# Optimization experiments

Measured on AMD Instinct MI355X. Metric: run time of the kernel, lower is better.

The kernel has to match this reference:

```python
import jax, jax.numpy as jnp
import numpy as np

H, HD, NKV = 16, 128, 4           # heads, head_dim, n_kv_heads (kv_groups=4)
SEL_TOPK, SEL_DIM, SEL_HEADS = 64, 64, 1
ROPE_BASE = 10000.0


def _rope_emb(t, hd):
    inv = 1.0 / (ROPE_BASE ** (jnp.arange(0, hd, 2, dtype=jnp.float32) / hd))
    freqs = jnp.arange(t, dtype=jnp.float32)[:, None] * inv[None, :]
    return jnp.concatenate([freqs, freqs], axis=-1)  # [t, hd]


def _apply_rotary(x, rope):
    # x: [b, t, h, hd]; rope: [t, hd] (rot_dim == hd here)
    cos = jnp.cos(rope)[None, :, None, :]
    sin = jnp.sin(rope)[None, :, None, :]
    x1, x2 = x[..., ::2], x[..., 1::2]
    c, s = cos[..., ::2], sin[..., ::2]
    rot = jnp.stack([x1 * c - x2 * s, x1 * s + x2 * c], axis=-1)
    return rot.reshape(x.shape)


def _selector_mask(q, k):
    # q, k: [b, H, t, hd] in UNrotated form (selector_rope='none'); causal=True
    b, h, t, d = q.shape
    qs = q[:, :SEL_HEADS, :, :SEL_DIM]
    ks = k[:, :SEL_HEADS, :, :SEL_DIM]
    scores = jnp.einsum('bhqd,bhkd->bhqk', qs, ks) / np.sqrt(SEL_DIM).astype(np.float32)
    future = jnp.triu(jnp.ones((t, t), bool), 1)
    scores = jnp.where(future[None, None], -jnp.inf, scores)
    idx = jax.lax.top_k(scores, SEL_TOPK)[1]  # [b, h_sel, t, keep]
    rows = jnp.arange(t)
    scatter_row = lambda im: jnp.zeros((t, t), bool).at[rows[:, None], im].set(True)
    sel = jax.vmap(jax.vmap(scatter_row))(idx)          # [b, h_sel, t, t]
    sel = sel.at[:, :, rows, rows].set(True)            # diagonal always kept
    sel = sel & jnp.tril(jnp.ones((t, t), bool))[None, None]
    sel = jnp.any(sel, axis=1, keepdims=True)           # h_sel < h -> broadcast mask
    return jnp.where(sel, 0.0, -jnp.inf).astype(jnp.float32)


def reference(x, Wq, bq, Wkd, bkd, Wku, bku, Wo, bo):
    b, t, d = x.shape
    G = H // NKV
    q = (x @ Wq + bq).reshape(b, t, H, HD)
    kv = (x @ Wkd + bkd) @ Wku + bku                    # MLA: down then up projection
    k = kv[..., : NKV * HD].reshape(b, t, NKV, HD)
    v = kv[..., NKV * HD:].reshape(b, t, NKV, HD)
    rope = _rope_emb(t, HD)
    qb = _apply_rotary(q, rope).transpose(0, 2, 1, 3)                     # [b,H,t,hd]
    kb = jnp.repeat(_apply_rotary(k, rope).transpose(0, 2, 1, 3), G, 1)   # GQA expand
    vb = jnp.repeat(v.transpose(0, 2, 1, 3), G, 1)
    # selector mask from unrotated q/k, detached (selector_detach=True)
    qu = jax.lax.stop_gradient(q.transpose(0, 2, 1, 3))
    ku = jnp.repeat(jax.lax.stop_gradient(k.transpose(0, 2, 1, 3)), G, 1)
    mask = _selector_mask(qu, ku)                                         # [b,1,t,t]
    scores = jnp.einsum('bhqd,bhkd->bhqk', qb, kb) / np.sqrt(HD).astype(np.float32)
    attn = jax.nn.softmax(scores + mask, axis=-1)
    y = jnp.einsum('bhqk,bhkd->bhqd', attn, vb)
    y = y.transpose(0, 2, 1, 3).reshape(b, t, H * HD)
    return y @ Wo + bo


def setup_inputs() -> dict:
    key = jax.random.key(0)
    ks = jax.random.split(key, 6)
    B, T, D, LAT = 2, 2048, 2048, 512
    s = 0.02
    return {
        'x': jax.random.normal(ks[0], (B, T, D), jnp.float32),
        'Wq': jax.random.normal(ks[1], (D, H * HD), jnp.float32) * s,
        'bq': jnp.zeros((H * HD,), jnp.float32),
        'Wkd': jax.random.normal(ks[2], (D, LAT), jnp.float32) * s,
        'bkd': jnp.zeros((LAT,), jnp.float32),
        'Wku': jax.random.normal(ks[3], (LAT, 2 * NKV * HD), jnp.float32) * s,
        'bku': jnp.zeros((2 * NKV * HD,), jnp.float32),
        'Wo': jax.random.normal(ks[4], (H * HD, D), jnp.float32) * s,
        'bo': jnp.zeros((D,), jnp.float32),
    }
```

## Files before the change

### kernel.cpp

```cpp
#include <hip/hip_runtime.h>

typedef unsigned int u32;
typedef unsigned long long u64;
typedef _Float16 f16;
typedef __attribute__((ext_vector_type(2))) _Float16 f16x2;
typedef __attribute__((ext_vector_type(4))) _Float16 f16x4;
typedef __attribute__((ext_vector_type(8))) _Float16 f16x8;
typedef __attribute__((ext_vector_type(4))) float f32x4;
typedef __attribute__((ext_vector_type(2))) double f64x2;


__device__ __forceinline__ int suX(int jj) { return jj ^ ((jj >> 4) & 7); }

__global__ __launch_bounds__(256) void k_transpose_cast(const float* __restrict__ in,
                                                        f16* __restrict__ out, int R, int C)
{
  __shared__ float tile[32][33];
  int c0 = blockIdx.x * 32, r0 = blockIdx.y * 32;
  int tx = threadIdx.x & 31, ty = threadIdx.x >> 5;
  #pragma unroll
  for (int i = ty; i < 32; i += 8) tile[i][tx] = in[(size_t)(r0 + i) * C + c0 + tx];
  __syncthreads();
  #pragma unroll
  for (int i = ty; i < 32; i += 8) out[(size_t)(c0 + i) * R + r0 + tx] = (f16)tile[tx][i];
}

__global__ __launch_bounds__(256) void k_cast_f16(const float* __restrict__ in,
                                                  f16* __restrict__ out, int n4)
{
  int i = blockIdx.x * 256 + threadIdx.x;
  if (i >= n4) return;
  f32x4 v = *(const f32x4*)&in[(size_t)i * 4];
  f16x4 h; h.x = (f16)v.x; h.y = (f16)v.y; h.z = (f16)v.z; h.w = (f16)v.w;
  *(f16x4*)&out[(size_t)i * 4] = h;
}

__global__ void k_prep_sel(const float* __restrict__ Wq, const float* __restrict__ Wkd,
                           const float* __restrict__ Wku, double* __restrict__ Bsel)
{
  const int k = blockIdx.x;
  const int j = threadIdx.x;
  Bsel[(size_t)k * 128 + j] = (double)Wq[(size_t)k * 2048 + j];
  double s = 0.0;
  for (int l = 0; l < 512; ++l)
    s = fma((double)Wkd[(size_t)k * 512 + l], (double)Wku[(size_t)l * 1024 + j], s);
  Bsel[(size_t)k * 128 + 64 + j] = s;
}

__global__ void k_bias_sel(const float* __restrict__ bq, const float* __restrict__ bkd,
                           const float* __restrict__ Wku, const float* __restrict__ bku,
                           double* __restrict__ bsel)
{
  int j = threadIdx.x;
  if (j < 64) {
    bsel[j] = (double)bq[j];
  } else {
    int jj = j - 64;
    double s = (double)bku[jj];
    for (int l = 0; l < 512; ++l)
      s = fma((double)bkd[l], (double)Wku[(size_t)l * 1024 + jj], s);
    bsel[j] = s;
  }
}

__global__ __launch_bounds__(256) void k_gemm_sel_f64(const float* __restrict__ A,
                                                      const double* __restrict__ Bsel,
                                                      double* __restrict__ partial)
{
  __shared__ double As[32][33];
  __shared__ double Bs[32][66];
  const int m0 = blockIdx.x * 32, n0 = blockIdx.y * 64;
  const int kbase = blockIdx.z * 512, kend = kbase + 512;
  const int tid = threadIdx.x;
  const int tx = tid & 15, ty = tid >> 4;
  const int ar = tid >> 3, ac4 = (tid & 7) * 4;
  double acc[2][4] = {};

  f32x4 aN = *(const f32x4*)&A[(size_t)(m0 + ar) * 2048 + kbase + ac4];
  f64x2 bN[4];
  #pragma unroll
  for (int it = 0; it < 4; ++it) {
    int c = it * 256 + tid; int kk = c >> 5, n2 = (c & 31) * 2;
    bN[it] = *(const f64x2*)&Bsel[(size_t)(kbase + kk) * 128 + n0 + n2];
  }
  for (int k0 = kbase; k0 < kend; k0 += 32) {
    __syncthreads();
    As[ar][ac4] = (double)aN.x; As[ar][ac4 + 1] = (double)aN.y;
    As[ar][ac4 + 2] = (double)aN.z; As[ar][ac4 + 3] = (double)aN.w;
    #pragma unroll
    for (int it = 0; it < 4; ++it) {
      int c = it * 256 + tid; int kk = c >> 5, n2 = (c & 31) * 2;
      Bs[kk][n2] = bN[it].x; Bs[kk][n2 + 1] = bN[it].y;
    }
    __syncthreads();
    if (k0 + 32 < kend) {
      aN = *(const f32x4*)&A[(size_t)(m0 + ar) * 2048 + k0 + 32 + ac4];
      #pragma unroll
      for (int it = 0; it < 4; ++it) {
        int c = it * 256 + tid; int kk = c >> 5, n2 = (c & 31) * 2;
        bN[it] = *(const f64x2*)&Bsel[(size_t)(k0 + 32 + kk) * 128 + n0 + n2];
      }
    }
    #pragma unroll
    for (int kk = 0; kk < 32; ++kk) {
      double a0 = As[ty * 2][kk], a1 = As[ty * 2 + 1][kk];
      f64x2 b01 = *(const f64x2*)&Bs[kk][tx * 4];
      f64x2 b23 = *(const f64x2*)&Bs[kk][tx * 4 + 2];
      acc[0][0] = fma(a0, b01.x, acc[0][0]); acc[0][1] = fma(a0, b01.y, acc[0][1]);
      acc[0][2] = fma(a0, b23.x, acc[0][2]); acc[0][3] = fma(a0, b23.y, acc[0][3]);
      acc[1][0] = fma(a1, b01.x, acc[1][0]); acc[1][1] = fma(a1, b01.y, acc[1][1]);
      acc[1][2] = fma(a1, b23.x, acc[1][2]); acc[1][3] = fma(a1, b23.y, acc[1][3]);
    }
  }
  double* op = partial + (size_t)blockIdx.z * 4096 * 128;
  #pragma unroll
  for (int i = 0; i < 2; ++i) {
    int row = m0 + ty * 2 + i;
    #pragma unroll
    for (int j = 0; j < 4; ++j) {
      int n = n0 + tx * 4 + j;
      op[(size_t)row * 128 + n] = acc[i][j];
    }
  }
}

__global__ __launch_bounds__(256) void k_sel_reduce(const double* __restrict__ partial,
                                                    const double* __restrict__ bias,
                                                    double* __restrict__ qs64,
                                                    double* __restrict__ ks64)
{
  const int idx = blockIdx.x * 256 + threadIdx.x;
  const int row = idx >> 7, n = idx & 127;
  const size_t S = 4096 * 128;
  double v = ((partial[idx] + partial[S + idx]) + partial[2 * S + idx]) + partial[3 * S + idx];
  v += bias[n];
  if (n < 64) qs64[(size_t)row * 64 + n] = v;
  else        ks64[(size_t)row * 64 + (n - 64)] = v;
}

__global__ __launch_bounds__(256) void k_transpose64(const double* __restrict__ in,
                                                     double* __restrict__ out)
{
  __shared__ double tile[32][33];
  const int bt = blockIdx.z;
  const int c0 = blockIdx.x * 32;
  const int r0 = blockIdx.y * 32;
  int tx = threadIdx.x & 31, ty = threadIdx.x >> 5;
  const double* ip = in + (size_t)bt * 2048 * 64;
  double* op = out + (size_t)bt * 64 * 2048;
  #pragma unroll
  for (int i = ty; i < 32; i += 8) tile[i][tx] = ip[(size_t)(r0 + i) * 64 + c0 + tx];
  __syncthreads();
  #pragma unroll
  for (int i = ty; i < 32; i += 8) op[(size_t)(c0 + i) * 2048 + r0 + tx] = tile[tx][i];
}

template <bool OUTF16>
__global__ __launch_bounds__(256) void k_gemm_bt(const f16* __restrict__ A,
                                                 const f16* __restrict__ BT,
                                                 const float* __restrict__ bias,
                                                 float* __restrict__ C, f16* __restrict__ Ch,
                                                 int M, int N, int K, int lda, int ldb, int ldc)
{
  __shared__ __align__(16) f16 As[128 * 64];
  __shared__ __align__(16) f16 Bs[128 * 64];
  const int tid = threadIdx.x;
  const int lane = tid & 63;
  const int wave = tid >> 6;
  const int m0 = blockIdx.x * 128, n0 = blockIdx.y * 128;
  const int wr = (wave >> 1) * 64, wc = (wave & 1) * 64;
  const int lrow = lane & 15;
  const int kgrp = (lane >> 4) * 8;
  f32x4 acc[4][4] = {};

  for (int k0 = 0; k0 < K; k0 += 64) {
    __syncthreads();
    #pragma unroll
    for (int it = 0; it < 4; ++it) {
      int c = it * 256 + tid;
      int r = c >> 3, c8 = (c & 7) * 8;
      int lbase = (it * 256 + (tid & 192)) * 8;
      const f16* ga = A + (size_t)(m0 + r) * lda + k0 + c8;
      __builtin_amdgcn_global_load_lds((const __attribute__((address_space(1))) u32*)ga,
                                       (__attribute__((address_space(3))) u32*)&As[lbase],
                                       16, 0, 0);
      const f16* gb = BT + (size_t)(n0 + r) * ldb + k0 + c8;
      __builtin_amdgcn_global_load_lds((const __attribute__((address_space(1))) u32*)gb,
                                       (__attribute__((address_space(3))) u32*)&Bs[lbase],
                                       16, 0, 0);
    }
    __syncthreads();
    #pragma unroll
    for (int ks = 0; ks < 2; ++ks) {
      f16x8 af[4], bfr[4];
      #pragma unroll
      for (int m = 0; m < 4; ++m)
        af[m] = *(const f16x8*)&As[(wr + m * 16 + lrow) * 64 + ks * 32 + kgrp];
      #pragma unroll
      for (int n = 0; n < 4; ++n)
        bfr[n] = *(const f16x8*)&Bs[(wc + n * 16 + lrow) * 64 + ks * 32 + kgrp];
      #pragma unroll
      for (int m = 0; m < 4; ++m)
        #pragma unroll
        for (int n = 0; n < 4; ++n)
          acc[m][n] = __builtin_amdgcn_mfma_f32_16x16x32_f16(af[m], bfr[n], acc[m][n], 0, 0, 0);
    }
  }
  const int rbase = m0 + wr + (lane >> 4) * 4;
  #pragma unroll
  for (int n = 0; n < 4; ++n) {
    int col = n0 + wc + n * 16 + lrow;
    float bv = bias ? bias[col] : 0.0f;
    #pragma unroll
    for (int m = 0; m < 4; ++m) {
      #pragma unroll
      for (int j = 0; j < 4; ++j) {
        int rowi = rbase + m * 16 + j;
        float v = acc[m][n][j] + bv;
        if (OUTF16) Ch[(size_t)rowi * ldc + col] = (f16)v;
        else        C[(size_t)rowi * ldc + col] = v;
      }
    }
  }
}

__global__ void k_rope_table(float* __restrict__ rc, float* __restrict__ rs)
{
  int t = blockIdx.x, i = threadIdx.x;
  int fi = (2 * i) & 63;
  double inv = pow(10000.0, -(double)fi / 64.0);
  double a = (double)t * inv;
  rc[t * 64 + i] = (float)cos(a);
  rs[t * 64 + i] = (float)sin(a);
}

__global__ __launch_bounds__(256) void k_rope_q(const f16* __restrict__ q,
                                                const float* __restrict__ rc,
                                                const float* __restrict__ rs,
                                                f16* __restrict__ out)
{
  int g = blockIdx.x * 256 + threadIdx.x;
  int row = g >> 10, rem = g & 1023;
  int h = rem >> 6, i = rem & 63;
  int t = row & 2047;
  size_t base = (size_t)row * 2048 + h * 128 + 2 * i;
  f16x2 v = *(const f16x2*)&q[base];
  float x1 = (float)v.x, x2 = (float)v.y;
  float c = rc[t * 64 + i], s = rs[t * 64 + i];
  f16x2 o; o.x = (f16)(x1 * c - x2 * s); o.y = (f16)(x1 * s + x2 * c);
  *(f16x2*)&out[base] = o;
}

__global__ __launch_bounds__(256) void k_rope_kv(const f16* __restrict__ kv,
                                                 const float* __restrict__ rc,
                                                 const float* __restrict__ rs,
                                                 f16* __restrict__ kout, f16* __restrict__ vout)
{
  int g = blockIdx.x * 256 + threadIdx.x;
  int row = g >> 8, rem = g & 255;
  int kvh = rem >> 6, i = rem & 63;
  int t = row & 2047;
  size_t kb = (size_t)row * 1024 + kvh * 128 + 2 * i;
  f16x2 kvp = *(const f16x2*)&kv[kb];
  float x1 = (float)kvp.x, x2 = (float)kvp.y;
  float c = rc[t * 64 + i], s = rs[t * 64 + i];
  size_t ob = (size_t)row * 512 + kvh * 128 + 2 * i;
  f16x2 ko; ko.x = (f16)(x1 * c - x2 * s); ko.y = (f16)(x1 * s + x2 * c);
  *(f16x2*)&kout[ob] = ko;
  f16x2 vp = *(const f16x2*)&kv[(size_t)row * 1024 + 512 + kvh * 128 + 2 * i];
  *(f16x2*)&vout[ob] = vp;
}

__global__ __launch_bounds__(256) void k_topk64(const double* __restrict__ qs,
                                                const double* __restrict__ ksT,
                                                int* __restrict__ selcnt,
                                                int* __restrict__ selidx)
{
  const int r0 = blockIdx.x * 2;
  const int b = r0 >> 11;
  const int t0 = r0 & 2047, t1 = t0 + 1;
  const int tid = threadIdx.x;
  if (t1 < 64) {
    for (int lr = 0; lr < 2; ++lr) {
      int t = t0 + lr;
      int* outp = selidx + (size_t)(r0 + lr) * 68;
      for (int jj = tid; jj <= t; jj += 256) outp[jj] = jj;
      if (tid == 0) selcnt[r0 + lr] = t + 1;
    }
    return;
  }
  __shared__ double qrowP[64][2];
  __shared__ u64 su[2][2048];
  __shared__ unsigned hist[256], sA[256], sB[256];
  __shared__ unsigned s_bsel, s_larger, s_cnt;
  __shared__ u64 s_thr;
  __shared__ int s_remfin;
  __shared__ int cand[128];
  __shared__ u64 ckey[128];

  if (tid < 128) qrowP[tid >> 1][tid & 1] = qs[(size_t)(r0 + (tid & 1)) * 64 + (tid >> 1)];
  __syncthreads();
  {
    const double* kb = ksT + (size_t)b * 64 * 2048;
    const int emax = t1 >> 8;
    for (int e = 0; e <= emax; ++e) {
      const int jj = e * 256 + tid;
      double acc0 = 0.0, acc1 = 0.0;
      const double* kp = kb + jj;
      #pragma unroll 16
      for (int d = 0; d < 64; ++d) {
        double kv = kp[(size_t)d * 2048];
        f64x2 qp = *(const f64x2*)&qrowP[d][0];
        acc0 = fma(qp.x, kv, acc0);
        acc1 = fma(qp.y, kv, acc1);
      }
      const int sx = suX(jj);
      u64 u0 = (u64)__double_as_longlong(acc0);
      su[0][sx] = (u0 >> 63) ? ~u0 : (u0 | 0x8000000000000000ull);
      u64 u1 = (u64)__double_as_longlong(acc1);
      su[1][sx] = (u1 >> 63) ? ~u1 : (u1 | 0x8000000000000000ull);
    }
  }
  __syncthreads();

  const int c0 = tid * 8;
  for (int lr = 0; lr < 2; ++lr) {
    const int t = t0 + lr;
    int* outp = selidx + (size_t)(r0 + lr) * 68;
    const u64* S = su[lr];
    u64 prefix = 0;
    int remaining = 64;
    int broke = 0, sh_final = 0;
    for (int byte = 7; byte >= 0; --byte) {
      const int sh = byte * 8;
      hist[tid] = 0;
      __syncthreads();
      {
        unsigned bn[8]; bool vl[8];
        #pragma unroll
        for (int e = 0; e < 8; ++e) {
          int jj = c0 + e;
          u64 u = (jj <= t) ? S[suX(jj)] : 0;
          bool ok = (jj <= t) && ((byte == 7) || (((u ^ prefix) >> (sh + 8)) == 0));
          bn[e] = (unsigned)((u >> sh) & 255);
          vl[e] = ok;
        }
        #pragma unroll
        for (int e = 0; e < 8; ++e) {
          if (vl[e]) {
            bool first = true;
            #pragma unroll
            for (int p = 0; p < 8; ++p)
              if (p < e && vl[p] && bn[p] == bn[e]) first = false;
            if (first) {
              unsigned c = 0;
              #pragma unroll
              for (int q = 0; q < 8; ++q)
                if (q >= e && vl[q] && bn[q] == bn[e]) ++c;
              atomicAdd(&hist[bn[e]], c);
            }
          }
        }
      }
      __syncthreads();
      unsigned* sp = sA; unsigned* dp = sB;
      sp[tid] = hist[tid];
      __syncthreads();
      #pragma unroll
      for (int off = 1; off < 256; off <<= 1) {
        dp[tid] = sp[tid] + ((tid + off < 256) ? sp[tid + off] : 0u);
        __syncthreads();
        unsigned* tpp = sp; sp = dp; dp = tpp;
      }
      unsigned inc = sp[tid];
      unsigned cumAbove = (tid == 255) ? 0u : sp[tid + 1];
      if ((int)cumAbove < remaining && (int)inc >= remaining) {
        s_bsel = (unsigned)tid;
        s_larger = cumAbove;
        s_cnt = inc - cumAbove;
      }
      __syncthreads();
      prefix |= ((u64)s_bsel << sh);
      remaining -= (int)s_larger;
      int cnt = (int)s_cnt;
      __syncthreads();
      if (cnt <= 128) { broke = 1; sh_final = sh; break; }
    }
    u64 thr;
    int remfin;
    if (broke) {
      unsigned cg = 0;
      #pragma unroll
      for (int e = 0; e < 8; ++e) {
        int jj = c0 + e;
        if (jj <= t && (((S[suX(jj)] ^ prefix) >> sh_final) == 0)) ++cg;
      }
      unsigned* sp = sA; unsigned* dp = sB;
      sp[tid] = cg;
      __syncthreads();
      #pragma unroll
      for (int off = 1; off < 256; off <<= 1) {
        dp[tid] = sp[tid] + ((tid >= off) ? sp[tid - off] : 0u);
        __syncthreads();
        unsigned* tpp = sp; sp = dp; dp = tpp;
      }
      const int C = (int)sp[255];
      int pos = (int)(sp[tid] - cg);
      #pragma unroll
      for (int e = 0; e < 8; ++e) {
        int jj = c0 + e;
        if (jj <= t && (((S[suX(jj)] ^ prefix) >> sh_final) == 0)) cand[pos++] = jj;
      }
      __syncthreads();
      if (tid < C) ckey[tid] = S[suX(cand[tid])];
      __syncthreads();
      if (tid < C) {
        u64 k = ckey[tid];
        int g = 0, eq = 0;
        for (int j = 0; j < C; ++j) {
          g += (ckey[j] > k) ? 1 : 0;
          eq += (ckey[j] == k) ? 1 : 0;
        }
        if (g < remaining && remaining <= g + eq) {
          s_thr = k;
          s_remfin = remaining - g;
        }
      }
      __syncthreads();
      thr = s_thr;
      remfin = s_remfin;
    } else {
      thr = prefix;
      remfin = remaining;
    }
    __syncthreads();
    unsigned cg = 0, ct_ = 0;
    #pragma unroll
    for (int e = 0; e < 8; ++e) {
      int jj = c0 + e;
      if (jj <= t) {
        u64 u = S[suX(jj)];
        cg += (u > thr) ? 1u : 0u;
        ct_ += (u == thr) ? 1u : 0u;
      }
    }
    const unsigned pack = cg | (ct_ << 16);
    {
      unsigned* sp = sA; unsigned* dp = sB;
      sp[tid] = pack;
      __syncthreads();
      #pragma unroll
      for (int off = 1; off < 256; off <<= 1) {
        dp[tid] = sp[tid] + ((tid >= off) ? sp[tid - off] : 0u);
        __syncthreads();
        unsigned* tpp = sp; sp = dp; dp = tpp;
      }
      const unsigned excl = sp[tid] - pack;
      const unsigned tot = sp[255];
      const unsigned Gtot = tot & 0xFFFFu;
      const u64 ut = S[suX(t)];
      const unsigned gt = (ut > thr) ? 1u : 0u;
      const unsigned tt = (ut == thr) ? 1u : 0u;
      const int GtotX = (int)(Gtot - gt);
      int gpos = (int)(excl & 0xFFFFu);
      int tpos = (int)(excl >> 16);
      #pragma unroll
      for (int e = 0; e < 8; ++e) {
        int jj = c0 + e;
        if (jj > t) break;
        u64 u = S[suX(jj)];
        if (u > thr) {
          if (jj != t) outp[1 + gpos] = jj;
          ++gpos;
        } else if (u == thr) {
          if (jj != t && tpos < remfin) outp[1 + GtotX + tpos] = jj;
          ++tpos;
        }
      }
      if (tid == 0) {
        outp[0] = t;
        const unsigned Ttot = tot >> 16;
        int tb = (int)(Ttot - tt);
        int emitT = tb < remfin ? tb : remfin;
        selcnt[r0 + lr] = 1 + GtotX + emitT;
      }
    }
    __syncthreads();
  }
}

__global__ __launch_bounds__(256) void k_attn(const f16* __restrict__ qr,
                                              const f16* __restrict__ kr,
                                              const f16* __restrict__ vv,
                                              const int* __restrict__ selcnt,
                                              const int* __restrict__ selidx,
                                              f16* __restrict__ y)
{
  const int blk = blockIdx.x;
  const int row = blk >> 2, kvh = blk & 3;
  const int b = row >> 11;
  const int tid = threadIdx.x, lane = tid & 63, wave = tid >> 6;
  const int cnt = selcnt[row];
  __shared__ int sidx[68];
  __shared__ __align__(16) f16 Kl[65 * 128];
  __shared__ __align__(16) f16 Vl[65 * 128];
  __shared__ f16 qlds[4][128];
  __shared__ float pl[4][66];
  if (tid < cnt) sidx[tid] = selidx[(size_t)row * 68 + tid];
  *(f16x2*)&qlds[wave][lane * 2] =
      *(const f16x2*)&qr[((size_t)row * 16 + kvh * 4 + wave) * 128 + lane * 2];
  __syncthreads();

  const int nch = cnt * 16;
  for (int c = tid; c < nch; c += 256) {
    const int r = c >> 4, ch = c & 15;
    const size_t kbase = ((size_t)(b * 2048 + sidx[r])) * 512 + kvh * 128 + ch * 8;
    f16x8 k8 = *(const f16x8*)&kr[kbase];
    *(f16x8*)&Kl[r * 128 + ((ch ^ (r & 15)) * 8)] = k8;
    f16x8 v8 = *(const f16x8*)&vv[kbase];
    *(f16x8*)&Vl[r * 128 + ch * 8] = v8;
  }
  __syncthreads();

  const float SCALE = 0.08838834764831845f;
  auto dotk = [&](int r) -> float {
    const int sw = r & 15;
    float s = 0.0f;
    #pragma unroll
    for (int i = 0; i < 16; ++i) {
      f16x8 k8 = *(const f16x8*)&Kl[r * 128 + ((i ^ sw) * 8)];
      f16x8 q8 = *(const f16x8*)&qlds[wave][i * 8];
      #pragma unroll
      for (int e = 0; e < 4; ++e) {
        f16x2 ka; ka.x = k8[2 * e]; ka.y = k8[2 * e + 1];
        f16x2 qa; qa.x = q8[2 * e]; qa.y = q8[2 * e + 1];
        s = __builtin_amdgcn_fdot2(ka, qa, s, false);
      }
    }
    return s * SCALE;
  };

  float s1 = -__builtin_inff(), s2 = -__builtin_inff();
  if (lane < cnt) s1 = dotk(lane);
  if (lane + 64 < cnt) s2 = dotk(lane + 64);
  float mx = fmaxf(s1, s2);
  #pragma unroll
  for (int off = 32; off; off >>= 1) mx = fmaxf(mx, __shfl_xor(mx, off));
  float p1 = (lane < cnt) ? __expf(s1 - mx) : 0.0f;
  float p2 = (lane + 64 < cnt) ? __expf(s2 - mx) : 0.0f;
  float l = p1 + p2;
  #pragma unroll
  for (int off = 32; off; off >>= 1) l += __shfl_xor(l, off);
  float linv = 1.0f / l;
  pl[wave][lane] = p1;
  if (lane == 0) pl[wave][64] = p2;
  __syncthreads();

  float y0 = 0.0f, y1 = 0.0f;
  const int d2 = lane * 2;
  for (int j = 0; j < cnt; ++j) {
    float p = pl[wave][j];
    f16x2 v2 = *(const f16x2*)&Vl[j * 128 + d2];
    y0 = fmaf(p, (float)v2.x, y0);
    y1 = fmaf(p, (float)v2.y, y1);
  }
  y0 *= linv; y1 *= linv;
  f16x2 o; o.x = (f16)y0; o.y = (f16)y1;
  *(f16x2*)&y[(size_t)row * 2048 + (kvh * 4 + wave) * 128 + d2] = o;
}

extern "C" void kernel_launch(void* const* d_in, const int* in_sizes, int n_in,
                              void* d_out, int out_size, void* d_ws, size_t ws_size,
                              hipStream_t stream)
{
  (void)in_sizes; (void)n_in; (void)out_size; (void)ws_size;
  const float* x   = (const float*)d_in[0];
  const float* Wq  = (const float*)d_in[1];
  const float* bq  = (const float*)d_in[2];
  const float* Wkd = (const float*)d_in[3];
  const float* bkd = (const float*)d_in[4];
  const float* Wku = (const float*)d_in[5];
  const float* bku = (const float*)d_in[6];
  const float* Wo  = (const float*)d_in[7];
  const float* bo  = (const float*)d_in[8];
  float* out = (float*)d_out;

  char* ws = (char*)d_ws;
  size_t o = 0;
  auto alloc = [&](size_t bytes) -> void* {
    o = (o + 255) & ~(size_t)255;
    void* p = ws + o;
    o += bytes;
    return p;
  };
  f16* WqT   = (f16*)alloc(2048ull * 2048 * 2);
  f16* WoT   = (f16*)alloc(2048ull * 2048 * 2);
  f16* WkdT  = (f16*)alloc(512ull * 2048 * 2);
  f16* WkuT  = (f16*)alloc(1024ull * 512 * 2);
  f16* xh    = (f16*)alloc(4096ull * 2048 * 2);
  f16* qmain = (f16*)alloc(4096ull * 2048 * 2);
  f16* kvh_  = (f16*)alloc(4096ull * 1024 * 2);
  f16* cbf   = (f16*)alloc(4096ull * 512 * 2);
  float* rc  = (float*)alloc(2048ull * 64 * 4);
  float* rs  = (float*)alloc(2048ull * 64 * 4);
  f16* qrope = (f16*)alloc(4096ull * 2048 * 2);
  f16* krope = (f16*)alloc(4096ull * 512 * 2);
  f16* vbf   = (f16*)alloc(4096ull * 512 * 2);
  int* selcnt = (int*)alloc(4096ull * 4);
  int* selidx = (int*)alloc(4096ull * 68 * 4);
  double* Bsel = (double*)alloc(2048ull * 128 * 8);
  double* bsel = (double*)alloc(128 * 8);
  double* qs64 = (double*)alloc(4096ull * 64 * 8);
  double* ks64 = (double*)alloc(4096ull * 64 * 8);
  double* ksT  = (double*)alloc(2ull * 64 * 2048 * 8);
  f16* yh = qmain;
  double* partial = (double*)qrope;

  k_transpose_cast<<<dim3(64, 64), 256, 0, stream>>>(Wq, WqT, 2048, 2048);
  k_transpose_cast<<<dim3(16, 64), 256, 0, stream>>>(Wkd, WkdT, 2048, 512);
  k_transpose_cast<<<dim3(32, 16), 256, 0, stream>>>(Wku, WkuT, 512, 1024);
  k_transpose_cast<<<dim3(64, 64), 256, 0, stream>>>(Wo, WoT, 2048, 2048);
  k_cast_f16<<<8192, 256, 0, stream>>>(x, xh, 2097152);

  k_prep_sel<<<2048, 64, 0, stream>>>(Wq, Wkd, Wku, Bsel);
  k_bias_sel<<<1, 128, 0, stream>>>(bq, bkd, Wku, bku, bsel);
  k_gemm_sel_f64<<<dim3(128, 2, 4), 256, 0, stream>>>(x, Bsel, partial);
  k_sel_reduce<<<2048, 256, 0, stream>>>(partial, bsel, qs64, ks64);
  k_transpose64<<<dim3(2, 64, 2), 256, 0, stream>>>(ks64, ksT);

  k_gemm_bt<true><<<dim3(32, 16), 256, 0, stream>>>(xh, WqT, bq, nullptr, qmain,
                                                    4096, 2048, 2048, 2048, 2048, 2048);
  k_gemm_bt<true><<<dim3(32, 4), 256, 0, stream>>>(xh, WkdT, bkd, nullptr, cbf,
                                                   4096, 512, 2048, 2048, 2048, 512);
  k_gemm_bt<true><<<dim3(32, 8), 256, 0, stream>>>(cbf, WkuT, bku, nullptr, kvh_,
                                                   4096, 1024, 512, 512, 512, 1024);

  k_rope_table<<<2048, 64, 0, stream>>>(rc, rs);
  k_rope_q<<<16384, 256, 0, stream>>>(qmain, rc, rs, qrope);
  k_rope_kv<<<4096, 256, 0, stream>>>(kvh_, rc, rs, krope, vbf);

  k_topk64<<<2048, 256, 0, stream>>>(qs64, ksT, selcnt, selidx);

  k_attn<<<16384, 256, 0, stream>>>(qrope, krope, vbf, selcnt, selidx, yh);

  k_gemm_bt<false><<<dim3(32, 16), 256, 0, stream>>>(yh, WoT, bo, out, nullptr,
                                                     4096, 2048, 2048, 2048, 2048, 2048);
}
```

Baseline: 537.9 us.

## Use MFMA for sparse attention QK and PV in k_attn

Rewrites the per-row sparse attention kernel to compute the 4 query heads of a KV group against the selected keys with 16x16x32 f16 MFMA instructions instead of per-lane fdot2 loops. V is held in registers, then transposed into the shared buffer that held K, with an XOR swizzle, so that P·V also runs on MFMA. Probabilities are normalized and stored as f16 in a padded buffer. This adds LDS transpose work, wastes 12 of the 16 MFMA rows, and lowers precision by rounding P to f16.

```diff
diff --git a/kernel.cpp b/kernel.cpp
--- a/kernel.cpp
+++ b/kernel.cpp
@@ -502,71 +502,129 @@
   const int tid = threadIdx.x, lane = tid & 63, wave = tid >> 6;
   const int cnt = selcnt[row];
   __shared__ int sidx[68];
-  __shared__ __align__(16) f16 Kl[65 * 128];
-  __shared__ __align__(16) f16 Vl[65 * 128];
-  __shared__ f16 qlds[4][128];
-  __shared__ float pl[4][66];
+  __shared__ __align__(16) f16 KV[13312];
+  __shared__ __align__(16) f16 Pbuf[16 * 104];
   if (tid < cnt) sidx[tid] = selidx[(size_t)row * 68 + tid];
-  *(f16x2*)&qlds[wave][lane * 2] =
-      *(const f16x2*)&qr[((size_t)row * 16 + kvh * 4 + wave) * 128 + lane * 2];
   __syncthreads();
 
-  const int nch = cnt * 16;
-  for (int c = tid; c < nch; c += 256) {
+  for (int c = tid; c < cnt * 16; c += 256) {
     const int r = c >> 4, ch = c & 15;
-    const size_t kbase = ((size_t)(b * 2048 + sidx[r])) * 512 + kvh * 128 + ch * 8;
-    f16x8 k8 = *(const f16x8*)&kr[kbase];
-    *(f16x8*)&Kl[r * 128 + ((ch ^ (r & 15)) * 8)] = k8;
-    f16x8 v8 = *(const f16x8*)&vv[kbase];
-    *(f16x8*)&Vl[r * 128 + ch * 8] = v8;
-  }
+    f16x8 k8 = *(const f16x8*)&kr[((size_t)(b * 2048 + sidx[r])) * 512 + kvh * 128 + ch * 8];
+    *(f16x8*)&KV[r * 128 + ((ch ^ (r & 15)) * 8)] = k8;
+  }
+  f16x8 vreg[6];
+  #pragma unroll
+  for (int it = 0; it < 6; ++it) {
+    const int c = it * 256 + tid;
+    const int r = c >> 4, ch = c & 15;
+    f16x8 z = {};
+    if (r < cnt)
+      z = *(const f16x8*)&vv[((size_t)(b * 2048 + sidx[r])) * 512 + kvh * 128 + ch * 8];
+    vreg[it] = z;
+  }
+  for (int i = tid; i < 16 * 104 / 2; i += 256) ((u32*)Pbuf)[i] = 0u;
+  const f16* qb = qr + (size_t)row * 2048 + (4 * kvh + (lane & 3)) * 128;
+  f16x8 qf[4];
+  #pragma unroll
+  for (int k0 = 0; k0 < 4; ++k0) qf[k0] = *(const f16x8*)&qb[k0 * 32 + (lane >> 4) * 8];
   __syncthreads();
 
+  f32x4 sc[5];
+  #pragma unroll
+  for (int n = 0; n < 5; ++n) {
+    f32x4 a = {0.f, 0.f, 0.f, 0.f};
+    const int r = n * 16 + (lane & 15);
+    #pragma unroll
+    for (int k0 = 0; k0 < 4; ++k0) {
+      const int ch = (k0 * 4 + (lane >> 4)) ^ (r & 15);
+      f16x8 bf = *(const f16x8*)&KV[r * 128 + ch * 8];
+      a = __builtin_amdgcn_mfma_f32_16x16x32_f16(qf[k0], bf, a, 0, 0, 0);
+    }
+    sc[n] = a;
+  }
   const float SCALE = 0.08838834764831845f;
-  auto dotk = [&](int r) -> float {
-    const int sw = r & 15;
-    float s = 0.0f;
-    #pragma unroll
-    for (int i = 0; i < 16; ++i) {
-      f16x8 k8 = *(const f16x8*)&Kl[r * 128 + ((i ^ sw) * 8)];
-      f16x8 q8 = *(const f16x8*)&qlds[wave][i * 8];
-      #pragma unroll
-      for (int e = 0; e < 4; ++e) {
-        f16x2 ka; ka.x = k8[2 * e]; ka.y = k8[2 * e + 1];
-        f16x2 qa; qa.x = q8[2 * e]; qa.y = q8[2 * e + 1];
-        s = __builtin_amdgcn_fdot2(ka, qa, s, false);
-      }
-    }
-    return s * SCALE;
-  };
-
-  float s1 = -__builtin_inff(), s2 = -__builtin_inff();
-  if (lane < cnt) s1 = dotk(lane);
-  if (lane + 64 < cnt) s2 = dotk(lane + 64);
-  float mx = fmaxf(s1, s2);
-  #pragma unroll
-  for (int off = 32; off; off >>= 1) mx = fmaxf(mx, __shfl_xor(mx, off));
-  float p1 = (lane < cnt) ? __expf(s1 - mx) : 0.0f;
-  float p2 = (lane + 64 < cnt) ? __expf(s2 - mx) : 0.0f;
-  float l = p1 + p2;
-  #pragma unroll
-  for (int off = 32; off; off >>= 1) l += __shfl_xor(l, off);
-  float linv = 1.0f / l;
-  pl[wave][lane] = p1;
-  if (lane == 0) pl[wave][64] = p2;
+  const float NINF = -__builtin_inff();
+  float ps[5][4];
+  float mx0 = NINF, mx1 = NINF, mx2 = NINF, mx3 = NINF;
+  #pragma unroll
+  for (int n = 0; n < 5; ++n) {
+    const bool ok = (n * 16 + (lane & 15)) < cnt;
+    #pragma unroll
+    for (int j = 0; j < 4; ++j) ps[n][j] = ok ? sc[n][j] * SCALE : NINF;
+    mx0 = fmaxf(mx0, ps[n][0]); mx1 = fmaxf(mx1, ps[n][1]);
+    mx2 = fmaxf(mx2, ps[n][2]); mx3 = fmaxf(mx3, ps[n][3]);
+  }
+  #pragma unroll
+  for (int off = 1; off < 16; off <<= 1) {
+    mx0 = fmaxf(mx0, __shfl_xor(mx0, off)); mx1 = fmaxf(mx1, __shfl_xor(mx1, off));
+    mx2 = fmaxf(mx2, __shfl_xor(mx2, off)); mx3 = fmaxf(mx3, __shfl_xor(mx3, off));
+  }
+  float l0 = 0.f, l1 = 0.f, l2 = 0.f, l3 = 0.f;
+  #pragma unroll
+  for (int n = 0; n < 5; ++n) {
+    ps[n][0] = __expf(ps[n][0] - mx0); l0 += ps[n][0];
+    ps[n][1] = __expf(ps[n][1] - mx1); l1 += ps[n][1];
+    ps[n][2] = __expf(ps[n][2] - mx2); l2 += ps[n][2];
+    ps[n][3] = __expf(ps[n][3] - mx3); l3 += ps[n][3];
+  }
+  #pragma unroll
+  for (int off = 1; off < 16; off <<= 1) {
+    l0 += __shfl_xor(l0, off); l1 += __shfl_xor(l1, off);
+    l2 += __shfl_xor(l2, off); l3 += __shfl_xor(l3, off);
+  }
+  const float i0 = 1.f / l0, i1 = 1.f / l1, i2 = 1.f / l2, i3 = 1.f / l3;
+  if (lane < 16) {
+    #pragma unroll
+    for (int n = 0; n < 5; ++n) {
+      const int key = n * 16 + lane;
+      Pbuf[0 * 104 + key] = (f16)(ps[n][0] * i0);
+      Pbuf[1 * 104 + key] = (f16)(ps[n][1] * i1);
+      Pbuf[2 * 104 + key] = (f16)(ps[n][2] * i2);
+      Pbuf[3 * 104 + key] = (f16)(ps[n][3] * i3);
+    }
+  }
   __syncthreads();
 
-  float y0 = 0.0f, y1 = 0.0f;
-  const int d2 = lane * 2;
-  for (int j = 0; j < cnt; ++j) {
-    float p = pl[wave][j];
-    f16x2 v2 = *(const f16x2*)&Vl[j * 128 + d2];
-    y0 = fmaf(p, (float)v2.x, y0);
-    y1 = fmaf(p, (float)v2.y, y1);
-  }
-  y0 *= linv; y1 *= linv;
-  f16x2 o; o.x = (f16)y0; o.y = (f16)y1;
-  *(f16x2*)&y[(size_t)row * 2048 + (kvh * 4 + wave) * 128 + d2] = o;
+  #pragma unroll
+  for (int it = 0; it < 6; ++it) {
+    const int c = it * 256 + tid;
+    const int r = c >> 4, ch = c & 15;
+    #pragma unroll
+    for (int e = 0; e < 8; ++e) {
+      const int d = ch * 8 + e;
+      const int rs = (r < 64) ? (r ^ (((d >> 3) & 7) << 3)) : r;
+      KV[d * 104 + rs] = vreg[it][e];
+    }
+  }
+  __syncthreads();
+
+  f32x4 ov0 = {0.f, 0.f, 0.f, 0.f}, ov1 = {0.f, 0.f, 0.f, 0.f};
+  #pragma unroll
+  for (int k0 = 0; k0 < 3; ++k0) {
+    f16x8 pa = *(const f16x8*)&Pbuf[(lane & 15) * 104 + k0 * 32 + (lane >> 4) * 8];
+    const int g = k0 * 4 + (lane >> 4);
+    const int rbase = g * 8;
+    {
+      const int d = wave * 32 + (lane & 15);
+      const int rs = (rbase < 64) ? (rbase ^ (((d >> 3) & 7) << 3)) : rbase;
+      f16x8 vb = *(const f16x8*)&KV[d * 104 + rs];
+      ov0 = __builtin_amdgcn_mfma_f32_16x16x32_f16(pa, vb, ov0, 0, 0, 0);
+    }
+    {
+      const int d = wave * 32 + 16 + (lane & 15);
+      const int rs = (rbase < 64) ? (rbase ^ (((d >> 3) & 7) << 3)) : rbase;
+      f16x8 vb = *(const f16x8*)&KV[d * 104 + rs];
+      ov1 = __builtin_amdgcn_mfma_f32_16x16x32_f16(pa, vb, ov1, 0, 0, 0);
+    }
+  }
+  if (lane < 16) {
+    const size_t yb = (size_t)row * 2048 + 4 * kvh * 128;
+    #pragma unroll
+    for (int j = 0; j < 4; ++j) {
+      y[yb + j * 128 + wave * 32 + lane] = (f16)ov0[j];
+      y[yb + j * 128 + wave * 32 + 16 + lane] = (f16)ov1[j];
+    }
+  }
 }
 
 extern "C" void kernel_launch(void* const* d_in, const int* in_sizes, int n_in,
```

New measurement: 591.3 us. +9.9%, slower.
